# Kernel optimization log

Measured on AMD Instinct MI355X. Metric: run time of the kernel, lower is better.

The kernel has to match this reference:

```python
import jax, jax.numpy as jnp
import numpy as np

B, N, D, H = 2, 384, 128, 8

def _ln(x, g, b, eps=1e-5):
    m = jnp.mean(x, -1, keepdims=True)
    v = jnp.mean((x - m) ** 2, -1, keepdims=True)
    return (x - m) * jax.lax.rsqrt(v + eps) * g + b

def _gelu(x):
    return jax.nn.gelu(x, approximate=False)  # torch nn.GELU default = exact erf

def setup_inputs() -> dict:
    key = jax.random.key(0)
    ks = jax.random.split(key, 20)
    def w(i, *s):
        return jax.random.normal(ks[i], s, jnp.float32) * 0.02
    return {
        'node_features': jax.random.normal(ks[0], (B, N, D), jnp.float32),
        'edge_features': jax.random.normal(ks[1], (B, N, N, D), jnp.float32),
        'mask': jnp.ones((B, N), dtype=bool),
        'attn_wqkv_node': w(2, D, 3 * D),
        'attn_wqkv_edge': w(3, D, 4 * D),
        'lin0_w': w(4, D, D), 'lin0_b': jnp.zeros(D, jnp.float32),
        'ln0_g': jnp.ones(D, jnp.float32), 'ln0_bias': jnp.zeros(D, jnp.float32),
        'ln1_g': jnp.ones(D, jnp.float32), 'ln1_bias': jnp.zeros(D, jnp.float32),
        'nmlp_w1': w(5, D, 2 * D), 'nmlp_w2': w(6, 2 * D, D), 'nmlp_b2': jnp.zeros(D, jnp.float32),
        'e0_we': w(7, 2 * D, D), 'e0_be': jnp.zeros(D, jnp.float32),
        'e0_ws': w(8, D, D), 'e0_bs': jnp.zeros(D, jnp.float32),
        'e0_wt': w(9, D, D), 'e0_bt': jnp.zeros(D, jnp.float32),
        'e0_wer': w(10, D, D), 'e0_wec': w(11, D, D),
        'e0_w1': w(12, D, D), 'e0_b1': jnp.zeros(D, jnp.float32),
        'e1_w1': w(13, D, 2 * D), 'e1_w2': w(14, 2 * D, D), 'e1_b2': jnp.zeros(D, jnp.float32),
        'eln0_g': jnp.ones(D, jnp.float32), 'eln0_b': jnp.zeros(D, jnp.float32),
        'eln1_g': jnp.ones(D, jnp.float32), 'eln1_b': jnp.zeros(D, jnp.float32),
    }

def _forward(node, edge, wqkv_n, wqkv_e, lin0_w, lin0_b, ln0_g, ln0_bias, ln1_g, ln1_bias,
             nmlp_w1, nmlp_w2, nmlp_b2, e0_we, e0_be, e0_ws, e0_bs, e0_wt, e0_bt,
             e0_wer, e0_wec, e0_w1, e0_b1, e1_w1, e1_w2, e1_b2, eln0_g, eln0_b, eln1_g, eln1_b):
    b, n, d = node.shape
    h = H
    dh = d // h
    scale = 1.0 / (d ** 0.5)  # note: scale uses full d_hid as in source
    # ---- RTAttention (modulate_v=True) ----
    qkv_n = (node @ wqkv_n).reshape(b, n, h, 3 * dh).transpose(0, 2, 1, 3)  # b h n 3dh
    qn, kn, vn = jnp.split(qkv_n, 3, axis=-1)
    qkv_e = (edge @ wqkv_e).reshape(b, n, n, h, 4 * dh).transpose(0, 3, 1, 2, 4)  # b h i j 4dh
    eq, ek, ev, em = jnp.split(qkv_e, 4, axis=-1)
    q = qn[:, :, :, None, :] + eq                      # b h i j dh
    k = kn[:, :, None, :, :] + ek
    v = vn[:, :, None, :, :] * em + ev                 # modulate_v: v_node*edge[3] + edge[2]
    dots = scale * jnp.einsum('bhijd,bhijd->bhij', q, k)
    attn = jax.nn.softmax(dots, axis=-1)
    out = jnp.einsum('bhij,bhijd->bhid', attn, v)
    out = out.transpose(0, 2, 1, 3).reshape(b, n, d)
    # ---- node updates, type 'rt' (dropout=0 -> identity) ----
    x = _ln(node + (out @ lin0_w + lin0_b), ln0_g, ln0_bias)
    x = _ln(x + (_gelu(x @ nmlp_w1) @ nmlp_w2 + nmlp_b2), ln1_g, ln1_bias)
    # ---- edge updates: EdgeMLP ----
    sn = (x @ e0_ws + e0_bs)[:, :, None, :]                       # broadcast over j
    tn = (x @ e0_wt + e0_bt)[:, None, :, :]                       # broadcast over i
    se = jnp.mean(edge, axis=1, keepdims=True) @ e0_wec           # mean over dim -3, lin0_ec
    te = jnp.mean(edge, axis=2, keepdims=True) @ e0_wer           # mean over dim -2, lin0_er
    e = jnp.concatenate([edge, jnp.swapaxes(edge, 1, 2)], axis=-1) @ e0_we + e0_be
    e = _gelu(e + sn + tn + se + te) @ e0_w1 + e0_b1
    edge2 = _ln(edge + e, eln0_g, eln0_b)
    edge2 = _ln(edge2 + (_gelu(edge2 @ e1_w1) @ e1_w2 + e1_b2), eln1_g, eln1_b)
    return x, edge2

def reference(node_features, edge_features, mask, attn_wqkv_node, attn_wqkv_edge,
              lin0_w, lin0_b, ln0_g, ln0_bias, ln1_g, ln1_bias,
              nmlp_w1, nmlp_w2, nmlp_b2, e0_we, e0_be, e0_ws, e0_bs, e0_wt, e0_bt,
              e0_wer, e0_wec, e0_w1, e0_b1, e1_w1, e1_w2, e1_b2,
              eln0_g, eln0_b, eln1_g, eln1_b):
    # mask is accepted but unused by the source forward path
    return _forward(node_features, edge_features, attn_wqkv_node, attn_wqkv_edge,
                    lin0_w, lin0_b, ln0_g, ln0_bias, ln1_g, ln1_bias,
                    nmlp_w1, nmlp_w2, nmlp_b2, e0_we, e0_be, e0_ws, e0_bs, e0_wt, e0_bt,
                    e0_wer, e0_wec, e0_w1, e0_b1, e1_w1, e1_w2, e1_b2,
                    eln0_g, eln0_b, eln1_g, eln1_b)
```

## Files before the change

kernel.cpp:

```cpp
#include <hip/hip_runtime.h>
#include <hip/hip_bf16.h>
#include <cstdint>
#include <cstddef>

#define B_ 2
#define N_ 384
#define D_ 128
#define NN (N_*N_)
#define BN (B_*N_)
#define EDGE_ELEMS (B_*NN*D_)
#define NODE_ELEMS (BN*D_)

typedef short bh8 __attribute__((ext_vector_type(8)));
typedef float f32x4 __attribute__((ext_vector_type(4)));

__device__ __forceinline__ f32x4 mfma_bf16(bh8 a, bh8 b, f32x4 c){
  return __builtin_amdgcn_mfma_f32_16x16x32_bf16(a, b, c, 0, 0, 0);
}
__device__ __forceinline__ unsigned short f2bf(float f){
  unsigned u = __float_as_uint(f);
  return (unsigned short)((u + 0x7fffu + ((u >> 16) & 1u)) >> 16);
}
__device__ __forceinline__ unsigned f2bf_pk(float a, float b){
  __hip_bfloat162 h = __float22bfloat162_rn(make_float2(a, b));
  return *(unsigned*)&h;
}
__device__ __forceinline__ float bf2f(unsigned short h){
  return __uint_as_float(((unsigned)h) << 16);
}
__device__ __forceinline__ float geluf(float x){
  return 0.5f * x * (1.0f + erff(x * 0.70710678118654752f));
}
__device__ __forceinline__ float gelu_fast(float x){
  float x2 = x * x;
  float t  = __fmaf_rn(0.044715f * x, x2, x);
  float e  = __expf(1.5957691216057308f * t);
  float r  = __builtin_amdgcn_rcpf(e + 1.0f);
  return x - x * r;
}
__device__ __forceinline__ f32x4 zero4(){ f32x4 z = {0.f,0.f,0.f,0.f}; return z; }

__device__ __forceinline__ float red16_add(float x){
  x += __int_as_float(__builtin_amdgcn_update_dpp(0, __float_as_int(x), 0xB1, 0xF, 0xF, true));
  x += __int_as_float(__builtin_amdgcn_update_dpp(0, __float_as_int(x), 0x4E, 0xF, 0xF, true));
  x += __int_as_float(__builtin_amdgcn_update_dpp(0, __float_as_int(x), 0x141, 0xF, 0xF, true));
  x += __int_as_float(__builtin_amdgcn_update_dpp(0, __float_as_int(x), 0x140, 0xF, 0xF, true));
  return x;
}
__device__ __forceinline__ float red4_add(float x){
  x += __int_as_float(__builtin_amdgcn_update_dpp(0, __float_as_int(x), 0xB1, 0xF, 0xF, true));
  x += __int_as_float(__builtin_amdgcn_update_dpp(0, __float_as_int(x), 0x4E, 0xF, 0xF, true));
  return x;
}
__device__ __forceinline__ int swz(int m, int p){
  return ((((p >> 3) ^ (m & 7)) << 3) | (p & 7));
}
__device__ __forceinline__ int PHIDX(int x){
  return (x & ~31) | ((x & 1) << 4) | ((x & 31) >> 1);
}

__global__ void kprep(const float* wqkv_e, const float* e0_we, const float* e0_w1,
                      const float* e1_w1, const float* e1_w2,
                      const float* node, const float* wqkv_n,
                      unsigned short* WqkvT, unsigned short* WeT, unsigned short* W1T,
                      unsigned short* E1W1T, unsigned short* E1W2T,
                      float* qkvn){
  int m = blockIdx.y;
  int tid = threadIdx.x;
  if (m < 5){
    const float* src; unsigned short* dst; int K, Nn;
    if (m == 0){ src = wqkv_e; dst = WqkvT; K = 128; Nn = 512; }
    else if (m == 1){ src = e0_we; dst = WeT;   K = 256; Nn = 128; }
    else if (m == 2){ src = e0_w1; dst = W1T;   K = 128; Nn = 128; }
    else if (m == 3){ src = e1_w1; dst = E1W1T; K = 128; Nn = 256; }
    else            { src = e1_w2; dst = E1W2T; K = 256; Nn = 128; }
    int idx = blockIdx.x * 384 + tid;
    if (idx < K * Nn){
      int n = idx / K, k = idx % K;
      int ksrc = (m >= 2) ? ((k & ~127) | PHIDX(k & 127)) : k;
      dst[idx] = f2bf(src[ksrc * Nn + n]);
    }
  } else {
    int row = blockIdx.x;
    __shared__ float sn[128];
    if (tid < 128) sn[tid] = node[row * 128 + tid];
    __syncthreads();
    float acc = 0.f;
    #pragma unroll 8
    for (int k = 0; k < 128; ++k) acc += sn[k] * wqkv_n[k * 384 + tid];
    qkvn[row * 384 + tid] = acc;
  }
}

__global__ void kprepA(const float* __restrict__ edge, unsigned short* __restrict__ E16,
                       float* __restrict__ meanJ){
  __shared__ float red[8][128];
  int bi = blockIdx.x; int tid = threadIdx.x;
  const float4* src = (const float4*)(edge + (size_t)bi * N_ * D_);
  uint2* gdst = (uint2*)E16 + (size_t)bi * (N_ * D_ / 4);
  float ps0 = 0.f, ps1 = 0.f, ps2 = 0.f, ps3 = 0.f;
  #pragma unroll 4
  for (int k = 0; k < 48; ++k){
    int idx = k * 256 + tid;
    float4 v = src[idx];
    uint2 o;
    o.x = f2bf_pk(v.x, v.y);
    o.y = f2bf_pk(v.z, v.w);
    gdst[idx] = o;
    ps0 += v.x; ps1 += v.y; ps2 += v.z; ps3 += v.w;
  }
  int g = tid >> 5, d0 = (tid & 31) * 4;
  red[g][d0] = ps0; red[g][d0 + 1] = ps1; red[g][d0 + 2] = ps2; red[g][d0 + 3] = ps3;
  __syncthreads();
  if (tid < 128){
    float s = 0.f;
    #pragma unroll
    for (int gg = 0; gg < 8; ++gg) s += red[gg][tid];
    meanJ[bi * 128 + tid] = s * (1.0f / N_);
  }
}

__global__ __launch_bounds__(256, 2) void kattnI(
    const unsigned short* __restrict__ E16, const unsigned short* __restrict__ WqkvT,
    const float* __restrict__ qkvn, float* __restrict__ attn,
    float* __restrict__ meanI){
  __shared__ float red[16][128];
  int tid = threadIdx.x;
  if (blockIdx.y == 1){
    int bj = blockIdx.x; int b = bj / N_, j = bj % N_;
    int ig = tid >> 4, dsub = tid & 15;
    float acc[8];
    #pragma unroll
    for (int e = 0; e < 8; ++e) acc[e] = 0.f;
    #pragma unroll 4
    for (int i = ig; i < N_; i += 16){
      const unsigned short* p = E16 + ((size_t)(b * N_ + i) * N_ + j) * D_ + dsub * 8;
      uint4 u = *(const uint4*)p;
      acc[0] += bf2f((unsigned short)(u.x & 0xffff)); acc[1] += bf2f((unsigned short)(u.x >> 16));
      acc[2] += bf2f((unsigned short)(u.y & 0xffff)); acc[3] += bf2f((unsigned short)(u.y >> 16));
      acc[4] += bf2f((unsigned short)(u.z & 0xffff)); acc[5] += bf2f((unsigned short)(u.z >> 16));
      acc[6] += bf2f((unsigned short)(u.w & 0xffff)); acc[7] += bf2f((unsigned short)(u.w >> 16));
    }
    #pragma unroll
    for (int e = 0; e < 8; ++e) red[ig][dsub * 8 + e] = acc[e];
    __syncthreads();
    if (tid < 128){
      float s = 0.f;
      #pragma unroll
      for (int gg = 0; gg < 16; ++gg) s += red[gg][tid];
      meanI[bj * 128 + tid] = s * (1.0f / N_);
    }
    return;
  }
  int bi = blockIdx.x; int b = bi / N_;
  int w = tid >> 6, lane = tid & 63, quad = lane >> 4, c16 = lane & 15;
  const float scale = 0.08838834764831845f;
  const unsigned short* Abase = E16 + (size_t)bi * N_ * D_;

  bh8 bf[2][4][4];
  #pragma unroll
  for (int s = 0; s < 2; ++s){
    int h = w + s * 4;
    #pragma unroll
    for (int u = 0; u < 4; ++u)
      #pragma unroll
      for (int ks = 0; ks < 4; ++ks){
        int col = h * 64 + u * 16 + c16;
        bf[s][u][ks] = *(const bh8*)(WqkvT + col * 128 + ks * 32 + quad * 8);
      }
  }
  float qv[2];
  #pragma unroll
  for (int s = 0; s < 2; ++s) qv[s] = qkvn[bi * 384 + (w + s * 4) * 48 + c16];

  float m_run[2] = {-1e30f, -1e30f}, l_run[2] = {0.f, 0.f}, o[2] = {0.f, 0.f};
  bh8 af[4];
  #pragma unroll
  for (int ks = 0; ks < 4; ++ks)
    af[ks] = *(const bh8*)(Abase + (size_t)c16 * D_ + ks * 32 + quad * 8);

  for (int jt = 0; jt < 24; ++jt){
    int jn = (jt + 1 < 24) ? jt + 1 : 0;
    bh8 afn[4];
    #pragma unroll
    for (int ks = 0; ks < 4; ++ks)
      afn[ks] = *(const bh8*)(Abase + (size_t)(jn * 16 + c16) * D_ + ks * 32 + quad * 8);
    float knv[2][4], vnv[2][4];
    const float* kvb = qkvn + ((size_t)b * N_ + jt * 16 + quad * 4) * 384;
    #pragma unroll
    for (int s = 0; s < 2; ++s)
      #pragma unroll
      for (int r = 0; r < 4; ++r){
        knv[s][r] = kvb[r * 384 + (w + s * 4) * 48 + 16 + c16];
        vnv[s][r] = kvb[r * 384 + (w + s * 4) * 48 + 32 + c16];
      }
    f32x4 EQ[2], EK[2], EV[2], EM[2];
    #pragma unroll
    for (int s = 0; s < 2; ++s){ EQ[s] = zero4(); EK[s] = zero4(); EV[s] = zero4(); EM[s] = zero4(); }
    #pragma unroll
    for (int ks = 0; ks < 4; ++ks)
      #pragma unroll
      for (int s = 0; s < 2; ++s){
        EQ[s] = mfma_bf16(af[ks], bf[s][0][ks], EQ[s]);
        EK[s] = mfma_bf16(af[ks], bf[s][1][ks], EK[s]);
        EV[s] = mfma_bf16(af[ks], bf[s][2][ks], EV[s]);
        EM[s] = mfma_bf16(af[ks], bf[s][3][ks], EM[s]);
      }
    #pragma unroll
    for (int s = 0; s < 2; ++s){
      float dots[4], vv[4];
      #pragma unroll
      for (int r = 0; r < 4; ++r){
        float t1 = (qv[s] + EQ[s][r]) * (knv[s][r] + EK[s][r]);
        dots[r] = red16_add(t1) * scale;
        vv[r] = vnv[s][r] * EM[s][r] + EV[s][r];
      }
      float tmax = fmaxf(fmaxf(dots[0], dots[1]), fmaxf(dots[2], dots[3]));
      tmax = fmaxf(tmax, __shfl_xor(tmax, 16));
      tmax = fmaxf(tmax, __shfl_xor(tmax, 32));
      float mnew = fmaxf(m_run[s], tmax);
      float al = __expf(m_run[s] - mnew);
      float p0 = __expf(dots[0] - mnew), p1 = __expf(dots[1] - mnew);
      float p2 = __expf(dots[2] - mnew), p3 = __expf(dots[3] - mnew);
      float lt = p0 + p1 + p2 + p3;
      lt += __shfl_xor(lt, 16); lt += __shfl_xor(lt, 32);
      l_run[s] = l_run[s] * al + lt;
      m_run[s] = mnew;
      o[s] = o[s] * al + p0 * vv[0] + p1 * vv[1] + p2 * vv[2] + p3 * vv[3];
    }
    #pragma unroll
    for (int ks = 0; ks < 4; ++ks) af[ks] = afn[ks];
  }
  #pragma unroll
  for (int s = 0; s < 2; ++s){
    float oo = o[s];
    oo += __shfl_xor(oo, 16); oo += __shfl_xor(oo, 32);
    oo /= l_run[s];
    if (quad == 0) attn[(size_t)bi * D_ + (w + s * 4) * 16 + c16] = oo;
  }
}

__global__ void knodeadd(const float* __restrict__ node, const float* __restrict__ attn,
                         const float* lin0_w, const float* lin0_b,
                         const float* g0, const float* bb0,
                         const float* w1, const float* w2, const float* b2,
                         const float* g1, const float* bb1,
                         const float* __restrict__ meanJ, const float* __restrict__ meanI,
                         const float* ws, const float* bs, const float* wt, const float* bt,
                         const float* wer, const float* wec, const float* be,
                         float* __restrict__ xOut,
                         float* __restrict__ rowAdd, float* __restrict__ colAdd){
  int row = blockIdx.x; int tid = threadIdx.x;
  __shared__ float sa[128], sx[128], sh[256], rb[8], sx2[128], smJ[128], smI[128];
  if (tid < 128){
    sa[tid] = attn[row * 128 + tid];
    smJ[tid] = meanJ[row * 128 + tid];
    smI[tid] = meanI[row * 128 + tid];
  }
  __syncthreads();
  float y = 0.f, x0 = 0.f;
  if (tid < 128){
    float acc = lin0_b[tid];
    #pragma unroll 8
    for (int k = 0; k < 128; ++k) acc += sa[k] * lin0_w[k * 128 + tid];
    y = acc + node[row * 128 + tid];
  }
  { float sv = (tid < 128) ? y : 0.f, sq = (tid < 128) ? y * y : 0.f;
    sv = red16_add(sv); sq = red16_add(sq);
    sv += __shfl_xor(sv, 16); sq += __shfl_xor(sq, 16);
    sv += __shfl_xor(sv, 32); sq += __shfl_xor(sq, 32);
    if ((tid & 63) == 0){ rb[tid >> 6] = sv; rb[4 + (tid >> 6)] = sq; } }
  __syncthreads();
  float mean = (rb[0] + rb[1] + rb[2] + rb[3]) * (1.f / 128.f);
  float var  = (rb[4] + rb[5] + rb[6] + rb[7]) * (1.f / 128.f) - mean * mean;
  float rstd = rsqrtf(var + 1e-5f);
  if (tid < 128){ x0 = (y - mean) * rstd * g0[tid] + bb0[tid]; sx[tid] = x0; }
  __syncthreads();
  { float acc = 0.f;
    #pragma unroll 8
    for (int k = 0; k < 128; ++k) acc += sx[k] * w1[k * 256 + tid];
    sh[tid] = geluf(acc); }
  __syncthreads();
  float y2 = 0.f;
  if (tid < 128){
    float acc = b2[tid];
    #pragma unroll 8
    for (int e = 0; e < 256; ++e) acc += sh[e] * w2[e * 128 + tid];
    y2 = acc + x0;
  }
  __syncthreads();
  { float sv = (tid < 128) ? y2 : 0.f, sq = (tid < 128) ? y2 * y2 : 0.f;
    sv = red16_add(sv); sq = red16_add(sq);
    sv += __shfl_xor(sv, 16); sq += __shfl_xor(sq, 16);
    sv += __shfl_xor(sv, 32); sq += __shfl_xor(sq, 32);
    if ((tid & 63) == 0){ rb[tid >> 6] = sv; rb[4 + (tid >> 6)] = sq; } }
  __syncthreads();
  mean = (rb[0] + rb[1] + rb[2] + rb[3]) * (1.f / 128.f);
  var  = (rb[4] + rb[5] + rb[6] + rb[7]) * (1.f / 128.f) - mean * mean;
  rstd = rsqrtf(var + 1e-5f);
  if (tid < 128){
    float xv = (y2 - mean) * rstd * g1[tid] + bb1[tid];
    xOut[row * 128 + tid] = xv;
    sx2[tid] = xv;
  }
  __syncthreads();
  if (tid < 128){
    int d = tid;
    float s1 = bs[d], s3 = 0.f;
    #pragma unroll 8
    for (int k = 0; k < 128; ++k){
      s1 += sx2[k] * ws[k * 128 + d];
      s3 += smJ[k] * wer[k * 128 + d];
    }
    rowAdd[row * 128 + d] = s1 + s3 + be[d];
  } else {
    int d = tid - 128;
    float s2 = bt[d], s4 = 0.f;
    #pragma unroll 8
    for (int k = 0; k < 128; ++k){
      s2 += sx2[k] * wt[k * 128 + d];
      s4 += smI[k] * wec[k * 128 + d];
    }
    colAdd[row * 128 + d] = s2 + s4;
  }
}

__global__ __launch_bounds__(256, 4) void kedge4(
    const unsigned short* __restrict__ E16, const unsigned short* __restrict__ WeT,
    const unsigned short* __restrict__ W1T, const unsigned short* __restrict__ E1W1T,
    const unsigned short* __restrict__ E1W2T,
    const float* __restrict__ rowAdd, const float* __restrict__ colAdd,
    const float* __restrict__ b1, const float* __restrict__ eg0, const float* __restrict__ eb0,
    const float* __restrict__ e1b2, const float* __restrict__ eg1, const float* __restrict__ eb1,
    float* __restrict__ eOut){
  __shared__ unsigned short sA[64][256];
#define HIFV(i) (((float*)&sA[0][0])[ (((i) >> 6) << 7) + 64 + ((i) & 63) ])
  int tid = threadIdx.x;
  int w = tid >> 6, lane = tid & 63, quad = lane >> 4, c16 = lane & 15;
  int R0 = blockIdx.x * 64;
  int b = R0 / NN; int rem = R0 % NN; int i = rem / N_; int j0 = rem % N_;

  bh8 wb1[2][8];
  #pragma unroll
  for (int t = 0; t < 2; ++t)
    #pragma unroll
    for (int ks = 0; ks < 8; ++ks){
      int col = w * 32 + t * 16 + c16;
      wb1[t][ks] = *(const bh8*)(WeT + (size_t)col * 256 + ks * 32 + quad * 8);
    }

  #pragma unroll
  for (int it = 0; it < 8; ++it){
    int cid = it * 256 + tid;
    int rrow = cid >> 5;
    int chunk = cid & 31;
    int kc = chunk * 8;
    const unsigned short* sp;
    if (kc < 128) sp = E16 + ((size_t)(b * N_ + i) * N_ + (j0 + rrow)) * D_ + kc;
    else          sp = E16 + ((size_t)(b * N_ + j0 + rrow) * N_ + i) * D_ + (kc - 128);
    *(float4*)&sA[rrow][(chunk ^ (rrow & 7)) << 3] = *(const float4*)sp;
  }
  __syncthreads();

  f32x4 acc1[2][4];
  #pragma unroll
  for (int t = 0; t < 2; ++t) for (int ms = 0; ms < 4; ++ms) acc1[t][ms] = zero4();
  #pragma unroll
  for (int ks = 0; ks < 8; ++ks){
    bh8 af[4];
    #pragma unroll
    for (int ms = 0; ms < 4; ++ms){
      int row = ms * 16 + c16;
      af[ms] = *(const bh8*)&sA[row][swz(row, ks * 32 + quad * 8)];
    }
    #pragma unroll
    for (int t = 0; t < 2; ++t)
      #pragma unroll
      for (int ms = 0; ms < 4; ++ms)
        acc1[t][ms] = mfma_bf16(af[ms], wb1[t][ks], acc1[t][ms]);
  }
  float rAv[2], ca[2][16];
  #pragma unroll
  for (int t = 0; t < 2; ++t){
    rAv[t] = rowAdd[(b * N_ + i) * D_ + w * 32 + t * 16 + c16];
    #pragma unroll
    for (int ms = 0; ms < 4; ++ms)
      #pragma unroll
      for (int r = 0; r < 4; ++r)
        ca[t][ms * 4 + r] = colAdd[(size_t)(b * N_ + j0 + ms * 16 + quad * 4 + r) * D_
                                   + w * 32 + t * 16 + c16];
  }
  __syncthreads();

  #pragma unroll
  for (int ms = 0; ms < 4; ++ms)
    #pragma unroll
    for (int r = 0; r < 4; ++r){
      int m = ms * 16 + quad * 4 + r;
      float v0 = gelu_fast(acc1[0][ms][r] + rAv[0] + ca[0][ms * 4 + r]);
      float v1 = gelu_fast(acc1[1][ms][r] + rAv[1] + ca[1][ms * 4 + r]);
      *(unsigned*)&sA[m][swz(m, 128 + w * 32 + c16 * 2)] = f2bf_pk(v0, v1);
    }
  __syncthreads();

  bh8 wb2[2][4];
  #pragma unroll
  for (int t = 0; t < 2; ++t)
    #pragma unroll
    for (int ks = 0; ks < 4; ++ks){
      int col = w * 32 + t * 16 + c16;
      wb2[t][ks] = *(const bh8*)(W1T + (size_t)col * 128 + ks * 32 + quad * 8);
    }
  f32x4 acc2[2][4];
  #pragma unroll
  for (int t = 0; t < 2; ++t) for (int ms = 0; ms < 4; ++ms) acc2[t][ms] = zero4();
  #pragma unroll
  for (int ks = 0; ks < 4; ++ks){
    bh8 af[4];
    #pragma unroll
    for (int ms = 0; ms < 4; ++ms){
      int row = ms * 16 + c16;
      af[ms] = *(const bh8*)&sA[row][swz(row, 128 + ks * 32 + quad * 8)];
    }
    #pragma unroll
    for (int t = 0; t < 2; ++t)
      #pragma unroll
      for (int ms = 0; ms < 4; ++ms)
        acc2[t][ms] = mfma_bf16(af[ms], wb2[t][ks], acc2[t][ms]);
  }
  float b1v[2], g0v[2], b0v[2];
  #pragma unroll
  for (int t = 0; t < 2; ++t){
    int c = w * 32 + t * 16 + c16;
    b1v[t] = b1[c]; g0v[t] = eg0[c]; b0v[t] = eb0[c];
  }
  __syncthreads();
  #pragma unroll
  for (int ms = 0; ms < 4; ++ms)
    #pragma unroll
    for (int r = 0; r < 4; ++r){
      int m = ms * 16 + quad * 4 + r;
      float s = 0.f, q = 0.f;
      #pragma unroll
      for (int t = 0; t < 2; ++t){
        float v = acc2[t][ms][r] + b1v[t] + bf2f(sA[m][swz(m, w * 32 + t * 16 + c16)]);
        acc2[t][ms][r] = v; s += v; q += v * v;
      }
      s = red16_add(s); q = red16_add(q);
      if (c16 == 0){ HIFV(w * 64 + m) = s; HIFV(256 + w * 64 + m) = q; }
    }
  __syncthreads();
  {
    int src = lane & 3, mrow = w * 16 + (lane >> 2);
    float sp = HIFV(src * 64 + mrow), qp = HIFV(256 + src * 64 + mrow);
    sp = red4_add(sp); qp = red4_add(qp);
    if (src == 0){
      float mean = sp * (1.f / 128.f);
      float var  = qp * (1.f / 128.f) - mean * mean;
      HIFV(512 + 2 * mrow) = mean;
      HIFV(513 + 2 * mrow) = rsqrtf(var + 1e-5f);
    }
  }
  __syncthreads();
  #pragma unroll
  for (int ms = 0; ms < 4; ++ms)
    #pragma unroll
    for (int r = 0; r < 4; ++r){
      int m = ms * 16 + quad * 4 + r;
      float2 st = *(float2*)&HIFV(512 + 2 * m);
      float e0 = (acc2[0][ms][r] - st.x) * st.y * g0v[0] + b0v[0];
      float e1 = (acc2[1][ms][r] - st.x) * st.y * g0v[1] + b0v[1];
      *(unsigned*)&sA[m][swz(m, w * 32 + c16 * 2)] = f2bf_pk(e0, e1);
    }
  __syncthreads();

  f32x4 acc4[2][4];
  #pragma unroll
  for (int t = 0; t < 2; ++t) for (int ms = 0; ms < 4; ++ms) acc4[t][ms] = zero4();
  #pragma unroll
  for (int p = 0; p < 2; ++p){
    bh8 wb3[2][4];
    #pragma unroll
    for (int t = 0; t < 2; ++t)
      #pragma unroll
      for (int ks = 0; ks < 4; ++ks){
        int col = p * 128 + w * 32 + t * 16 + c16;
        wb3[t][ks] = *(const bh8*)(E1W1T + (size_t)col * 128 + ks * 32 + quad * 8);
      }
    f32x4 acc3[2][4];
    #pragma unroll
    for (int t = 0; t < 2; ++t) for (int ms = 0; ms < 4; ++ms) acc3[t][ms] = zero4();
    #pragma unroll
    for (int ks = 0; ks < 4; ++ks){
      bh8 af[4];
      #pragma unroll
      for (int ms = 0; ms < 4; ++ms){
        int row = ms * 16 + c16;
        af[ms] = *(const bh8*)&sA[row][swz(row, ks * 32 + quad * 8)];
      }
      #pragma unroll
      for (int t = 0; t < 2; ++t)
        #pragma unroll
        for (int ms = 0; ms < 4; ++ms)
          acc3[t][ms] = mfma_bf16(af[ms], wb3[t][ks], acc3[t][ms]);
    }
    #pragma unroll
    for (int ms = 0; ms < 4; ++ms)
      #pragma unroll
      for (int r = 0; r < 4; ++r){
        int m = ms * 16 + quad * 4 + r;
        float v0 = gelu_fast(acc3[0][ms][r]);
        float v1 = gelu_fast(acc3[1][ms][r]);
        *(unsigned*)&sA[m][swz(m, 128 + w * 32 + c16 * 2)] = f2bf_pk(v0, v1);
      }
    __syncthreads();
    bh8 wb4[2][4];
    #pragma unroll
    for (int t = 0; t < 2; ++t)
      #pragma unroll
      for (int k2 = 0; k2 < 4; ++k2){
        int pcol = w * 32 + c16 * 2 + t;
        wb4[t][k2] = *(const bh8*)(E1W2T + (size_t)pcol * 256 + p * 128 + k2 * 32 + quad * 8);
      }
    #pragma unroll
    for (int k2 = 0; k2 < 4; ++k2){
      bh8 af[4];
      #pragma unroll
      for (int ms = 0; ms < 4; ++ms){
        int row = ms * 16 + c16;
        af[ms] = *(const bh8*)&sA[row][swz(row, 128 + k2 * 32 + quad * 8)];
      }
      #pragma unroll
      for (int t = 0; t < 2; ++t)
        #pragma unroll
        for (int ms = 0; ms < 4; ++ms)
          acc4[t][ms] = mfma_bf16(af[ms], wb4[t][k2], acc4[t][ms]);
    }
    __syncthreads();
  }

  float b2v[2], g1v[2], bb1v[2]; int slv[2];
  #pragma unroll
  for (int t = 0; t < 2; ++t){
    int pcol = w * 32 + c16 * 2 + t;
    b2v[t] = e1b2[pcol]; g1v[t] = eg1[pcol]; bb1v[t] = eb1[pcol];
    int lo5 = c16 * 2 + t;
    slv[t] = w * 32 + (((lo5 & 15) << 1) | (lo5 >> 4));
  }
  #pragma unroll
  for (int ms = 0; ms < 4; ++ms)
    #pragma unroll
    for (int r = 0; r < 4; ++r){
      int m = ms * 16 + quad * 4 + r;
      float s = 0.f, q = 0.f;
      #pragma unroll
      for (int t = 0; t < 2; ++t){
        float v = acc4[t][ms][r] + b2v[t] + bf2f(sA[m][swz(m, slv[t])]);
        acc4[t][ms][r] = v; s += v; q += v * v;
      }
      s = red16_add(s); q = red16_add(q);
      if (c16 == 0){ HIFV(w * 64 + m) = s; HIFV(256 + w * 64 + m) = q; }
    }
  __syncthreads();
  {
    int src = lane & 3, mrow = w * 16 + (lane >> 2);
    float sp = HIFV(src * 64 + mrow), qp = HIFV(256 + src * 64 + mrow);
    sp = red4_add(sp); qp = red4_add(qp);
    if (src == 0){
      float mean = sp * (1.f / 128.f);
      float var  = qp * (1.f / 128.f) - mean * mean;
      HIFV(512 + 2 * mrow) = mean;
      HIFV(513 + 2 * mrow) = rsqrtf(var + 1e-5f);
    }
  }
  __syncthreads();
  float* outBase = eOut + ((size_t)(b * N_ + i) * N_ + j0) * D_;
  #pragma unroll
  for (int ms = 0; ms < 4; ++ms)
    #pragma unroll
    for (int r = 0; r < 4; ++r){
      int m = ms * 16 + quad * 4 + r;
      float2 st = *(float2*)&HIFV(512 + 2 * m);
      float2 ov;
      ov.x = (acc4[0][ms][r] - st.x) * st.y * g1v[0] + bb1v[0];
      ov.y = (acc4[1][ms][r] - st.x) * st.y * g1v[1] + bb1v[1];
      *(float2*)&outBase[(size_t)m * D_ + w * 32 + c16 * 2] = ov;
    }
#undef HIFV
}

extern "C" void kernel_launch(void* const* d_in, const int* in_sizes, int n_in,
                              void* d_out, int out_size, void* d_ws, size_t ws_size,
                              hipStream_t stream){
  const float* node   = (const float*)d_in[0];
  const float* edge   = (const float*)d_in[1];
  const float* wqkv_n = (const float*)d_in[3];
  const float* wqkv_e = (const float*)d_in[4];
  const float* lin0_w = (const float*)d_in[5];
  const float* lin0_b = (const float*)d_in[6];
  const float* ln0_g  = (const float*)d_in[7];
  const float* ln0_b  = (const float*)d_in[8];
  const float* ln1_g  = (const float*)d_in[9];
  const float* ln1_b  = (const float*)d_in[10];
  const float* nmlp_w1= (const float*)d_in[11];
  const float* nmlp_w2= (const float*)d_in[12];
  const float* nmlp_b2= (const float*)d_in[13];
  const float* e0_we  = (const float*)d_in[14];
  const float* e0_be  = (const float*)d_in[15];
  const float* e0_ws  = (const float*)d_in[16];
  const float* e0_bs  = (const float*)d_in[17];
  const float* e0_wt  = (const float*)d_in[18];
  const float* e0_bt  = (const float*)d_in[19];
  const float* e0_wer = (const float*)d_in[20];
  const float* e0_wec = (const float*)d_in[21];
  const float* e0_w1  = (const float*)d_in[22];
  const float* e0_b1  = (const float*)d_in[23];
  const float* e1_w1  = (const float*)d_in[24];
  const float* e1_w2  = (const float*)d_in[25];
  const float* e1_b2  = (const float*)d_in[26];
  const float* eln0_g = (const float*)d_in[27];
  const float* eln0_b = (const float*)d_in[28];
  const float* eln1_g = (const float*)d_in[29];
  const float* eln1_b = (const float*)d_in[30];

  unsigned short* E16   = (unsigned short*)d_ws;
  unsigned short* WqkvT = E16 + (size_t)EDGE_ELEMS;
  unsigned short* WeT   = WqkvT + 65536;
  unsigned short* W1T   = WeT + 32768;
  unsigned short* E1W1T = W1T + 16384;
  unsigned short* E1W2T = E1W1T + 32768;
  float* fbase  = (float*)(E1W2T + 32768);
  float* qkvn   = fbase;
  float* attn   = qkvn + (size_t)BN * 384;
  float* meanJ  = attn + NODE_ELEMS;
  float* meanI  = meanJ + NODE_ELEMS;
  float* rowAdd = meanI + NODE_ELEMS;
  float* colAdd = rowAdd + NODE_ELEMS;

  float* xOut = (float*)d_out;
  float* eOut = xOut + NODE_ELEMS;

  kprep<<<dim3(BN, 6), 384, 0, stream>>>(wqkv_e, e0_we, e0_w1, e1_w1, e1_w2,
                                         node, wqkv_n,
                                         WqkvT, WeT, W1T, E1W1T, E1W2T, qkvn);
  kprepA<<<BN, 256, 0, stream>>>(edge, E16, meanJ);
  kattnI<<<dim3(BN, 2), 256, 0, stream>>>(E16, WqkvT, qkvn, attn, meanI);
  knodeadd<<<BN, 256, 0, stream>>>(node, attn, lin0_w, lin0_b, ln0_g, ln0_b,
                                   nmlp_w1, nmlp_w2, nmlp_b2, ln1_g, ln1_b,
                                   meanJ, meanI, e0_ws, e0_bs, e0_wt, e0_bt,
                                   e0_wer, e0_wec, e0_be,
                                   xOut, rowAdd, colAdd);
  kedge4<<<NN * B_ / 64, 256, 0, stream>>>(E16, WeT, W1T, E1W1T, E1W2T,
                                           rowAdd, colAdd, e0_b1,
                                           eln0_g, eln0_b, e1_b2, eln1_g, eln1_b,
                                           eOut);
}
```

Baseline: 657.1 us.

## Fuse edge bf16 conversion into prep kernel, process two rows per node block

Merges the edge fp32-to-bf16 conversion and column-mean pass (kprepA) into kprep as a seventh grid slice using 384 threads, removing one kernel launch and letting it run alongside the weight transposes. The node MLP kernel now processes two rows per 256-thread block so all threads do work in the LayerNorm and MLP stages, halving its grid. The edge kernel's launch bounds drop from 4 to 3 waves per SIMD, giving the compiler more registers at the cost of occupancy.

```diff
diff --git a/kernel.cpp b/kernel.cpp
--- a/kernel.cpp
+++ b/kernel.cpp
@@ -62,9 +62,11 @@
 __global__ void kprep(const float* wqkv_e, const float* e0_we, const float* e0_w1,
                       const float* e1_w1, const float* e1_w2,
                       const float* node, const float* wqkv_n,
+                      const float* __restrict__ edge,
                       unsigned short* WqkvT, unsigned short* WeT, unsigned short* W1T,
                       unsigned short* E1W1T, unsigned short* E1W2T,
-                      float* qkvn){
+                      float* qkvn, unsigned short* __restrict__ E16,
+                      float* __restrict__ meanJ){
   int m = blockIdx.y;
   int tid = threadIdx.x;
   if (m < 5){
@@ -80,7 +82,7 @@
       int ksrc = (m >= 2) ? ((k & ~127) | PHIDX(k & 127)) : k;
       dst[idx] = f2bf(src[ksrc * Nn + n]);
     }
-  } else {
+  } else if (m == 5){
     int row = blockIdx.x;
     __shared__ float sn[128];
     if (tid < 128) sn[tid] = node[row * 128 + tid];
@@ -89,34 +91,31 @@
     #pragma unroll 8
     for (int k = 0; k < 128; ++k) acc += sn[k] * wqkv_n[k * 384 + tid];
     qkvn[row * 384 + tid] = acc;
-  }
-}
-
-__global__ void kprepA(const float* __restrict__ edge, unsigned short* __restrict__ E16,
-                       float* __restrict__ meanJ){
-  __shared__ float red[8][128];
-  int bi = blockIdx.x; int tid = threadIdx.x;
-  const float4* src = (const float4*)(edge + (size_t)bi * N_ * D_);
-  uint2* gdst = (uint2*)E16 + (size_t)bi * (N_ * D_ / 4);
-  float ps0 = 0.f, ps1 = 0.f, ps2 = 0.f, ps3 = 0.f;
-  #pragma unroll 4
-  for (int k = 0; k < 48; ++k){
-    int idx = k * 256 + tid;
-    float4 v = src[idx];
-    uint2 o;
-    o.x = f2bf_pk(v.x, v.y);
-    o.y = f2bf_pk(v.z, v.w);
-    gdst[idx] = o;
-    ps0 += v.x; ps1 += v.y; ps2 += v.z; ps3 += v.w;
-  }
-  int g = tid >> 5, d0 = (tid & 31) * 4;
-  red[g][d0] = ps0; red[g][d0 + 1] = ps1; red[g][d0 + 2] = ps2; red[g][d0 + 3] = ps3;
-  __syncthreads();
-  if (tid < 128){
-    float s = 0.f;
-    #pragma unroll
-    for (int gg = 0; gg < 8; ++gg) s += red[gg][tid];
-    meanJ[bi * 128 + tid] = s * (1.0f / N_);
+  } else {
+    __shared__ float red[12][128];
+    int bi = blockIdx.x;
+    const float4* src = (const float4*)(edge + (size_t)bi * N_ * D_);
+    uint2* gdst = (uint2*)E16 + (size_t)bi * (N_ * D_ / 4);
+    float ps0 = 0.f, ps1 = 0.f, ps2 = 0.f, ps3 = 0.f;
+    #pragma unroll 4
+    for (int k = 0; k < 32; ++k){
+      int idx = k * 384 + tid;
+      float4 v = src[idx];
+      uint2 o;
+      o.x = f2bf_pk(v.x, v.y);
+      o.y = f2bf_pk(v.z, v.w);
+      gdst[idx] = o;
+      ps0 += v.x; ps1 += v.y; ps2 += v.z; ps3 += v.w;
+    }
+    int g = tid >> 5, d0 = (tid & 31) * 4;
+    red[g][d0] = ps0; red[g][d0 + 1] = ps1; red[g][d0 + 2] = ps2; red[g][d0 + 3] = ps3;
+    __syncthreads();
+    if (tid < 128){
+      float s = 0.f;
+      #pragma unroll
+      for (int gg = 0; gg < 12; ++gg) s += red[gg][tid];
+      meanJ[bi * 128 + tid] = s * (1.0f / N_);
+    }
   }
 }
 
@@ -250,82 +249,89 @@
                          const float* wer, const float* wec, const float* be,
                          float* __restrict__ xOut,
                          float* __restrict__ rowAdd, float* __restrict__ colAdd){
-  int row = blockIdx.x; int tid = threadIdx.x;
-  __shared__ float sa[128], sx[128], sh[256], rb[8], sx2[128], smJ[128], smI[128];
-  if (tid < 128){
-    sa[tid] = attn[row * 128 + tid];
-    smJ[tid] = meanJ[row * 128 + tid];
-    smI[tid] = meanI[row * 128 + tid];
-  }
-  __syncthreads();
-  float y = 0.f, x0 = 0.f;
-  if (tid < 128){
-    float acc = lin0_b[tid];
+  int tid = threadIdx.x;
+  int h = tid >> 7, lid = tid & 127;
+  int row = blockIdx.x * 2 + h;
+  __shared__ float sa[2][128], sx[2][128], sh[2][256], rb[8], sx2[2][128], smJ[2][128], smI[2][128];
+  sa[h][lid]  = attn[row * 128 + lid];
+  smJ[h][lid] = meanJ[row * 128 + lid];
+  smI[h][lid] = meanI[row * 128 + lid];
+  __syncthreads();
+  float y, x0;
+  {
+    float acc = lin0_b[lid];
     #pragma unroll 8
-    for (int k = 0; k < 128; ++k) acc += sa[k] * lin0_w[k * 128 + tid];
-    y = acc + node[row * 128 + tid];
-  }
-  { float sv = (tid < 128) ? y : 0.f, sq = (tid < 128) ? y * y : 0.f;
+    for (int k = 0; k < 128; ++k) acc += sa[h][k] * lin0_w[k * 128 + lid];
+    y = acc + node[row * 128 + lid];
+  }
+  { float sv = y, sq = y * y;
     sv = red16_add(sv); sq = red16_add(sq);
     sv += __shfl_xor(sv, 16); sq += __shfl_xor(sq, 16);
     sv += __shfl_xor(sv, 32); sq += __shfl_xor(sq, 32);
     if ((tid & 63) == 0){ rb[tid >> 6] = sv; rb[4 + (tid >> 6)] = sq; } }
   __syncthreads();
-  float mean = (rb[0] + rb[1] + rb[2] + rb[3]) * (1.f / 128.f);
-  float var  = (rb[4] + rb[5] + rb[6] + rb[7]) * (1.f / 128.f) - mean * mean;
+  float mean = (rb[h * 2] + rb[h * 2 + 1]) * (1.f / 128.f);
+  float var  = (rb[4 + h * 2] + rb[4 + h * 2 + 1]) * (1.f / 128.f) - mean * mean;
   float rstd = rsqrtf(var + 1e-5f);
-  if (tid < 128){ x0 = (y - mean) * rstd * g0[tid] + bb0[tid]; sx[tid] = x0; }
-  __syncthreads();
-  { float acc = 0.f;
+  x0 = (y - mean) * rstd * g0[lid] + bb0[lid];
+  sx[h][lid] = x0;
+  __syncthreads();
+  #pragma unroll
+  for (int u = 0; u < 2; ++u){
+    int e = lid + u * 128;
+    float acc = 0.f;
     #pragma unroll 8
-    for (int k = 0; k < 128; ++k) acc += sx[k] * w1[k * 256 + tid];
-    sh[tid] = geluf(acc); }
-  __syncthreads();
-  float y2 = 0.f;
-  if (tid < 128){
-    float acc = b2[tid];
+    for (int k = 0; k < 128; ++k) acc += sx[h][k] * w1[k * 256 + e];
+    sh[h][e] = geluf(acc);
+  }
+  __syncthreads();
+  float y2;
+  {
+    float acc = b2[lid];
     #pragma unroll 8
-    for (int e = 0; e < 256; ++e) acc += sh[e] * w2[e * 128 + tid];
+    for (int e = 0; e < 256; ++e) acc += sh[h][e] * w2[e * 128 + lid];
     y2 = acc + x0;
   }
-  __syncthreads();
-  { float sv = (tid < 128) ? y2 : 0.f, sq = (tid < 128) ? y2 * y2 : 0.f;
+  { float sv = y2, sq = y2 * y2;
     sv = red16_add(sv); sq = red16_add(sq);
     sv += __shfl_xor(sv, 16); sq += __shfl_xor(sq, 16);
     sv += __shfl_xor(sv, 32); sq += __shfl_xor(sq, 32);
     if ((tid & 63) == 0){ rb[tid >> 6] = sv; rb[4 + (tid >> 6)] = sq; } }
   __syncthreads();
-  mean = (rb[0] + rb[1] + rb[2] + rb[3]) * (1.f / 128.f);
-  var  = (rb[4] + rb[5] + rb[6] + rb[7]) * (1.f / 128.f) - mean * mean;
+  mean = (rb[h * 2] + rb[h * 2 + 1]) * (1.f / 128.f);
+  var  = (rb[4 + h * 2] + rb[4 + h * 2 + 1]) * (1.f / 128.f) - mean * mean;
   rstd = rsqrtf(var + 1e-5f);
-  if (tid < 128){
-    float xv = (y2 - mean) * rstd * g1[tid] + bb1[tid];
-    xOut[row * 128 + tid] = xv;
-    sx2[tid] = xv;
-  }
-  __syncthreads();
-  if (tid < 128){
-    int d = tid;
-    float s1 = bs[d], s3 = 0.f;
-    #pragma unroll 8
-    for (int k = 0; k < 128; ++k){
-      s1 += sx2[k] * ws[k * 128 + d];
-      s3 += smJ[k] * wer[k * 128 + d];
-    }
-    rowAdd[row * 128 + d] = s1 + s3 + be[d];
-  } else {
-    int d = tid - 128;
-    float s2 = bt[d], s4 = 0.f;
-    #pragma unroll 8
-    for (int k = 0; k < 128; ++k){
-      s2 += sx2[k] * wt[k * 128 + d];
-      s4 += smI[k] * wec[k * 128 + d];
-    }
-    colAdd[row * 128 + d] = s2 + s4;
-  }
-}
-
-__global__ __launch_bounds__(256, 4) void kedge4(
+  {
+    float xv = (y2 - mean) * rstd * g1[lid] + bb1[lid];
+    xOut[row * 128 + lid] = xv;
+    sx2[h][lid] = xv;
+  }
+  __syncthreads();
+  #pragma unroll
+  for (int rr = 0; rr < 2; ++rr){
+    int orow = blockIdx.x * 2 + rr;
+    int d = lid;
+    if (tid < 128){
+      float s1 = bs[d], s3 = 0.f;
+      #pragma unroll 8
+      for (int k = 0; k < 128; ++k){
+        s1 += sx2[rr][k] * ws[k * 128 + d];
+        s3 += smJ[rr][k] * wer[k * 128 + d];
+      }
+      rowAdd[orow * 128 + d] = s1 + s3 + be[d];
+    } else {
+      float s2 = bt[d], s4 = 0.f;
+      #pragma unroll 8
+      for (int k = 0; k < 128; ++k){
+        s2 += sx2[rr][k] * wt[k * 128 + d];
+        s4 += smI[rr][k] * wec[k * 128 + d];
+      }
+      colAdd[orow * 128 + d] = s2 + s4;
+    }
+  }
+}
+
+__global__ __launch_bounds__(256, 3) void kedge4(
     const unsigned short* __restrict__ E16, const unsigned short* __restrict__ WeT,
     const unsigned short* __restrict__ W1T, const unsigned short* __restrict__ E1W1T,
     const unsigned short* __restrict__ E1W2T,
@@ -640,16 +646,16 @@
   float* xOut = (float*)d_out;
   float* eOut = xOut + NODE_ELEMS;
 
-  kprep<<<dim3(BN, 6), 384, 0, stream>>>(wqkv_e, e0_we, e0_w1, e1_w1, e1_w2,
-                                         node, wqkv_n,
-                                         WqkvT, WeT, W1T, E1W1T, E1W2T, qkvn);
-  kprepA<<<BN, 256, 0, stream>>>(edge, E16, meanJ);
+  kprep<<<dim3(BN, 7), 384, 0, stream>>>(wqkv_e, e0_we, e0_w1, e1_w1, e1_w2,
+                                         node, wqkv_n, edge,
+                                         WqkvT, WeT, W1T, E1W1T, E1W2T,
+                                         qkvn, E16, meanJ);
   kattnI<<<dim3(BN, 2), 256, 0, stream>>>(E16, WqkvT, qkvn, attn, meanI);
-  knodeadd<<<BN, 256, 0, stream>>>(node, attn, lin0_w, lin0_b, ln0_g, ln0_b,
-                                   nmlp_w1, nmlp_w2, nmlp_b2, ln1_g, ln1_b,
-                                   meanJ, meanI, e0_ws, e0_bs, e0_wt, e0_bt,
-                                   e0_wer, e0_wec, e0_be,
-                                   xOut, rowAdd, colAdd);
+  knodeadd<<<BN / 2, 256, 0, stream>>>(node, attn, lin0_w, lin0_b, ln0_g, ln0_b,
+                                       nmlp_w1, nmlp_w2, nmlp_b2, ln1_g, ln1_b,
+                                       meanJ, meanI, e0_ws, e0_bs, e0_wt, e0_bt,
+                                       e0_wer, e0_wec, e0_be,
+                                       xOut, rowAdd, colAdd);
   kedge4<<<NN * B_ / 64, 256, 0, stream>>>(E16, WeT, W1T, E1W1T, E1W2T,
                                            rowAdd, colAdd, e0_b1,
                                            eln0_g, eln0_b, e1_b2, eln1_g, eln1_b,
```

Measured after the change: 623.6 us. -5.1%, faster.
